# Optimization experiments

Hardware: AMD Instinct MI355X
Metric: run time of the kernel (lower is better)

## Reference

```python
import jax, jax.numpy as jnp
import numpy as np

B, S, D_IN = 2, 2048, 1024
H, DA, DH = 16, 64, 64          # num_heads, attention_dim, head_dim (linear_hidden_dim)
EMBED = 1024
KSIZE = 1


def causal_conv1d(x_bsc, w):
    """x_bsc: (B,S,Cin); w: (Cout,Cin,K). Left-pad K-1 -> causal. Returns (B,Cout,S)."""
    k = w.shape[-1]
    x_bcs = jnp.transpose(x_bsc, (0, 2, 1))
    x_bcs = jnp.pad(x_bcs, ((0, 0), (0, 0), (k - 1, 0)))
    return jax.lax.conv_general_dilated(
        x_bcs, w, window_strides=(1,), padding='VALID',
        dimension_numbers=('NCH', 'OIH', 'NCH'))


def setup_inputs() -> dict:
    key = jax.random.key(0)
    ks = jax.random.split(key, 7)
    x = jax.random.normal(ks[0], (B, S, D_IN), dtype=jnp.float32)
    # causal mask: 1 where attended, 0 where masked (masked_fill where ==0)
    attn_mask = jnp.tril(jnp.ones((S, S), dtype=jnp.int32))[None, None]  # (1,1,S,S)
    wq = 0.02 * jax.random.normal(ks[1], (H * DA, D_IN, KSIZE), dtype=jnp.float32)
    wk = 0.02 * jax.random.normal(ks[2], (H * DA, D_IN, KSIZE), dtype=jnp.float32)
    wv = 0.02 * jax.random.normal(ks[3], (H * DH, D_IN, KSIZE), dtype=jnp.float32)
    w_out = 0.02 * jax.random.normal(ks[4], (EMBED, H * DH), dtype=jnp.float32)
    b_out = 0.02 * jax.random.normal(ks[5], (EMBED,), dtype=jnp.float32)
    return {"x": x, "attn_mask": attn_mask, "wq": wq, "wk": wk, "wv": wv,
            "w_out": w_out, "b_out": b_out}


def reference(x, attn_mask, wq, wk, wv, w_out, b_out):
    b, s, _ = x.shape
    scale = DH ** (-0.5)  # NOTE: torch code scales by head_dim, not attention_dim
    q = causal_conv1d(x, wq)  # (B, H*DA, S)
    k = causal_conv1d(x, wk)  # (B, H*DA, S)
    v = causal_conv1d(x, wv)  # (B, H*DH, S)
    q = q.reshape(b, H, DA, s).transpose(0, 1, 3, 2)  # (B,H,S,DA)
    k = k.reshape(b, H, DA, s).transpose(0, 1, 3, 2)
    v = v.reshape(b, H, DH, s).transpose(0, 1, 3, 2)  # (B,H,S,DH)
    scores = scale * jnp.einsum('bhnd,bhmd->bhnm', q, k)
    scores = jnp.where(attn_mask == 0, -jnp.inf, scores)
    probs = jax.nn.softmax(scores, axis=-1)
    context = jnp.einsum('bhnm,bhmd->bhnd', probs, v)  # (B,H,S,DH)
    context = context.transpose(0, 2, 1, 3).reshape(b, s, H * DH)
    return context @ w_out.T + b_out
```

## Files before the change

kernel.cpp:

```cpp
#include <hip/hip_runtime.h>
#include <math.h>


typedef __bf16 bf16;
typedef __bf16 bf16x8 __attribute__((ext_vector_type(8)));
typedef __bf16 bf16x4 __attribute__((ext_vector_type(4)));
typedef float  f32x4  __attribute__((ext_vector_type(4)));

#define MFMA16(a, b, c) __builtin_amdgcn_mfma_f32_16x16x32_bf16((a), (b), (c), 0, 0, 0)

__device__ __forceinline__ void gll16(const void* g, void* l) {
    __builtin_amdgcn_global_load_lds(
        (__attribute__((address_space(1))) unsigned int*)g,
        (__attribute__((address_space(3))) unsigned int*)l, 16, 0, 0);
}

__global__ __launch_bounds__(256) void cvt_all_kernel(
    const float* __restrict__ x,  const float* __restrict__ wq,
    const float* __restrict__ wk, const float* __restrict__ wv,
    const float* __restrict__ wo,
    bf16* __restrict__ xb,  bf16* __restrict__ wqb, bf16* __restrict__ wkb,
    bf16* __restrict__ wvb, bf16* __restrict__ wob)
{
    const int blk = blockIdx.x;
    const float* src; bf16* dst; int off; float scale = 1.f;
    if (blk < 4096)      { src = x;  dst = xb;  off = blk * 1024; }
    else if (blk < 5120) { src = wq; dst = wqb; off = (blk - 4096) * 1024;
                           scale = 0.18033688011112042f; }
    else if (blk < 6144) { src = wk; dst = wkb; off = (blk - 5120) * 1024; }
    else if (blk < 7168) { src = wv; dst = wvb; off = (blk - 6144) * 1024; }
    else                 { src = wo; dst = wob; off = (blk - 7168) * 1024; }
    const int i = off + threadIdx.x * 4;
    f32x4 v = *(const f32x4*)(src + i);
    bf16x4 o;
    o[0] = (bf16)(v[0] * scale); o[1] = (bf16)(v[1] * scale);
    o[2] = (bf16)(v[2] * scale); o[3] = (bf16)(v[3] * scale);
    *(bf16x4*)(dst + i) = o;
}

__global__ __launch_bounds__(256, 3) void qkv_mfma_kernel(
    const bf16* __restrict__ xb, const bf16* __restrict__ wqb,
    const bf16* __restrict__ wkb, const bf16* __restrict__ wvb,
    bf16* __restrict__ Qb, bf16* __restrict__ Kb, bf16* __restrict__ Vtb)
{
    __shared__ bf16 As[2][128 * 32];
    __shared__ bf16 Bs[2][128 * 32];
    const int mt = blockIdx.x;
    const int nt = blockIdx.y;
    const int which = nt >> 3;
    const bf16* Wm = (which == 0) ? wqb : (which == 1) ? wkb : wvb;

    const int t = threadIdx.x;
    const int w = t >> 6, lane = t & 63, quad = lane >> 4, l16 = lane & 15;
    const int wm = (w >> 1) * 64, wn = (w & 1) * 64;
    const int srow = lane >> 2;
    const int scol = (lane & 3) * 8;

    const bf16* Ab = xb + ((size_t)(mt * 128) + srow) * 1024 + scol;
    const bf16* Bb = Wm + ((size_t)((nt & 7) * 128) + srow) * 1024 + scol;

    f32x4 acc[4][4];
    #pragma unroll
    for (int i = 0; i < 4; i++)
        #pragma unroll
        for (int j = 0; j < 4; j++)
            #pragma unroll
            for (int r = 0; r < 4; r++) acc[i][j][r] = 0.f;

    gll16(Ab + (size_t)(w * 16) * 1024,       As[0] + w * 512);
    gll16(Ab + (size_t)((w + 4) * 16) * 1024, As[0] + (w + 4) * 512);
    gll16(Bb + (size_t)(w * 16) * 1024,       Bs[0] + w * 512);
    gll16(Bb + (size_t)((w + 4) * 16) * 1024, Bs[0] + (w + 4) * 512);

    for (int it = 0; it < 32; it++) {
        const int cur = it & 1, nxt = cur ^ 1;
        __syncthreads();
        if (it < 31) {
            const int kn = it * 32 + 32;
            gll16(Ab + (size_t)(w * 16) * 1024 + kn,       As[nxt] + w * 512);
            gll16(Ab + (size_t)((w + 4) * 16) * 1024 + kn, As[nxt] + (w + 4) * 512);
            gll16(Bb + (size_t)(w * 16) * 1024 + kn,       Bs[nxt] + w * 512);
            gll16(Bb + (size_t)((w + 4) * 16) * 1024 + kn, Bs[nxt] + (w + 4) * 512);
        }
        bf16x8 af[4], bfr[4];
        #pragma unroll
        for (int i = 0; i < 4; i++)
            af[i] = *(const bf16x8*)&As[cur][(wm + i * 16 + l16) * 32 + quad * 8];
        #pragma unroll
        for (int j = 0; j < 4; j++)
            bfr[j] = *(const bf16x8*)&Bs[cur][(wn + j * 16 + l16) * 32 + quad * 8];
        #pragma unroll
        for (int i = 0; i < 4; i++)
            #pragma unroll
            for (int j = 0; j < 4; j++)
                acc[i][j] = MFMA16(af[i], bfr[j], acc[i][j]);
    }

    const int nbase = (nt & 7) * 128 + wn;
    if (which == 2) {
        #pragma unroll
        for (int i = 0; i < 4; i++) {
            const int m0 = mt * 128 + wm + i * 16 + quad * 4;
            const int bb = m0 >> 11, s0 = m0 & 2047;
            #pragma unroll
            for (int j = 0; j < 4; j++) {
                const int n = nbase + j * 16 + l16;
                const int h = n >> 6, d = n & 63;
                bf16x4 pk;
                #pragma unroll
                for (int r = 0; r < 4; r++) pk[r] = (bf16)acc[i][j][r];
                *(bf16x4*)&Vtb[(((size_t)(bb * 16 + h)) * 64 + d) * 2048 + s0] = pk;
            }
        }
    } else {
        bf16* Out = (which == 0) ? Qb : Kb;
        #pragma unroll
        for (int i = 0; i < 4; i++) {
            #pragma unroll
            for (int r = 0; r < 4; r++) {
                const int m = mt * 128 + wm + i * 16 + quad * 4 + r;
                const int bb = m >> 11, s = m & 2047;
                #pragma unroll
                for (int j = 0; j < 4; j++) {
                    const int n = nbase + j * 16 + l16;
                    const int h = n >> 6, d = n & 63;
                    Out[(((size_t)(bb * 16 + h)) * 2048 + s) * 64 + d] =
                        (bf16)acc[i][j][r];
                }
            }
        }
    }
}

__global__ __launch_bounds__(256, 2) void attn_mfma_kernel(
    const bf16* __restrict__ Qb, const bf16* __restrict__ Kb,
    const bf16* __restrict__ Vtb, bf16* __restrict__ ctxb)
{
    __shared__ bf16 Ks[2][128 * 64];
    __shared__ bf16 Vts[2][64 * 128];
    __shared__ bf16 Pl[4][16 * 128];

    const int id = blockIdx.x;
    const int bh = id & 31;
    const int pr = id >> 5;
    const int qa = pr, qb = 31 - pr;
    const int h = bh & 15, b = bh >> 4;
    const int t = threadIdx.x;
    const int w = t >> 6, lane = t & 63, quad = lane >> 4, l16 = lane & 15;

    const size_t hb = (size_t)(b * 16 + h);
    const bf16* Qh = Qb + hb * (2048 * 64);
    const bf16* Kh = Kb + hb * (2048 * 64);
    const bf16* Vh = Vtb + hb * (64 * 2048);

    bf16x8 qf0[2], qf1[2];
    {
        const bf16* Qr0 = Qh + (size_t)(qa * 64 + w * 16 + l16) * 64;
        qf0[0] = *(const bf16x8*)(Qr0 + quad * 8);
        qf0[1] = *(const bf16x8*)(Qr0 + 32 + quad * 8);
        const bf16* Qr1 = Qh + (size_t)(qb * 64 + w * 16 + l16) * 64;
        qf1[0] = *(const bf16x8*)(Qr1 + quad * 8);
        qf1[1] = *(const bf16x8*)(Qr1 + 32 + quad * 8);
    }

    bf16x8 ones;
    #pragma unroll
    for (int i = 0; i < 8; i++) ones[i] = (bf16)1.0f;

    f32x4 o0[4], o1[4], l0, l1;
    #pragma unroll
    for (int r = 0; r < 4; r++) { l0[r] = 0.f; l1[r] = 0.f; }
    #pragma unroll
    for (int dt = 0; dt < 4; dt++)
        #pragma unroll
        for (int r = 0; r < 4; r++) { o0[dt][r] = 0.f; o1[dt][r] = 0.f; }

    const int ksr = lane >> 3, ksc = lane & 7;
    const int vsr = lane >> 4, vsc = lane & 15;

    #define STAGE(ktv, buf)                                                   \
        {                                                                     \
            _Pragma("unroll")                                                 \
            for (int j = 0; j < 4; j++) {                                     \
                const int c = 4 * w + j;                                      \
                const int kr = c * 8 + ksr;                                   \
                gll16(Kh + (size_t)((ktv) * 128 + kr) * 64 +                  \
                          ((ksc ^ (kr & 7)) * 8),                             \
                      Ks[buf] + c * 512);                                     \
                const int vr = c * 4 + vsr;                                   \
                gll16(Vh + (size_t)vr * 2048 + (ktv) * 128 +                  \
                          ((vsc ^ (vr & 15)) * 8),                            \
                      Vts[buf] + c * 512);                                    \
            }                                                                 \
        }

    #define ITER(qt64, ktv, diag, qfv, oacc, lacc, cur)                       \
        {                                                                     \
            f32x4 sacc[8];                                                    \
            _Pragma("unroll")                                                 \
            for (int tt = 0; tt < 8; tt++) {                                  \
                _Pragma("unroll")                                             \
                for (int r = 0; r < 4; r++) sacc[tt][r] = 0.f;                \
                const int krow = tt * 16 + l16;                               \
                bf16x8 kf0 = *(const bf16x8*)&Ks[cur][krow * 64 +             \
                                 ((quad)     ^ (krow & 7)) * 8];              \
                bf16x8 kf1 = *(const bf16x8*)&Ks[cur][krow * 64 +             \
                                 ((quad + 4) ^ (krow & 7)) * 8];              \
                sacc[tt] = MFMA16(kf0, (qfv)[0], sacc[tt]);                   \
                sacc[tt] = MFMA16(kf1, (qfv)[1], sacc[tt]);                   \
            }                                                                 \
            const int qrow = (qt64) * 64 + w * 16 + l16;                      \
            _Pragma("unroll")                                                 \
            for (int tt = 0; tt < 8; tt++) {                                  \
                bf16x4 pk;                                                    \
                _Pragma("unroll")                                             \
                for (int r = 0; r < 4; r++) {                                 \
                    float p = __builtin_amdgcn_exp2f(sacc[tt][r]);            \
                    if ((diag) && ((ktv) * 128 + tt * 16 + quad * 4 + r) > qrow) \
                        p = 0.f;                                              \
                    pk[r] = (bf16)p;                                          \
                }                                                             \
                const int cs = (tt * 2 + (quad >> 1)) ^ l16;                  \
                *(bf16x4*)&Pl[w][l16 * 128 + cs * 8 + (quad & 1) * 4] = pk;   \
            }                                                                 \
            bf16x8 ap[4];                                                     \
            _Pragma("unroll")                                                 \
            for (int u = 0; u < 4; u++) {                                     \
                ap[u] = *(const bf16x8*)&Pl[w][l16 * 128 +                    \
                             ((quad + 4 * u) ^ l16) * 8];                     \
                (lacc) = MFMA16(ap[u], ones, (lacc));                         \
            }                                                                 \
            _Pragma("unroll")                                                 \
            for (int dt = 0; dt < 4; dt++) {                                  \
                const int drow = dt * 16 + l16;                               \
                _Pragma("unroll")                                             \
                for (int u = 0; u < 4; u++) {                                 \
                    bf16x8 bv = *(const bf16x8*)&Vts[cur][drow * 128 +        \
                                     ((4 * u + quad) ^ (drow & 15)) * 8];     \
                    (oacc)[dt] = MFMA16(ap[u], bv, (oacc)[dt]);               \
                }                                                             \
            }                                                                 \
        }

    const int na = (qa >> 1) + 1;
    STAGE(0, 0);

    for (int v = 0; v < 17; v++) {
        const int cur = v & 1, nxt = cur ^ 1;
        __syncthreads();
        if (v < 16) {
            const int vn = v + 1;
            const int ktn = (vn < na) ? vn : vn - na;
            STAGE(ktn, nxt);
        }
        if (v < na) {
            ITER(qa, v, (v == na - 1), qf0, o0, l0, cur);
        } else {
            const int kt = v - na;
            ITER(qb, kt, (v == 16), qf1, o1, l1, cur);
        }
    }
    #undef STAGE
    #undef ITER

    #pragma unroll
    for (int r = 0; r < 4; r++) {
        const float inv0 = 1.f / l0[r];
        const int s0 = qa * 64 + w * 16 + quad * 4 + r;
        const float inv1 = 1.f / l1[r];
        const int s1 = qb * 64 + w * 16 + quad * 4 + r;
        #pragma unroll
        for (int dt = 0; dt < 4; dt++) {
            ctxb[((size_t)(b * 2048 + s0)) * 1024 + h * 64 + dt * 16 + l16] =
                (bf16)(o0[dt][r] * inv0);
            ctxb[((size_t)(b * 2048 + s1)) * 1024 + h * 64 + dt * 16 + l16] =
                (bf16)(o1[dt][r] * inv1);
        }
    }
}

__global__ __launch_bounds__(256, 2) void oproj_mfma_kernel(
    const bf16* __restrict__ ctxb, const bf16* __restrict__ wob,
    const float* __restrict__ b_out, float* __restrict__ out)
{
    __shared__ bf16 As[2][64 * 32];
    __shared__ bf16 Bs[2][128 * 32];
    const int mt = blockIdx.x;
    const int nt = blockIdx.y;
    const int t = threadIdx.x;
    const int w = t >> 6, lane = t & 63, quad = lane >> 4, l16 = lane & 15;
    const int srow = lane >> 2;
    const int scol = (lane & 3) * 8;

    const bf16* Ab = ctxb + (size_t)(mt * 64 + srow) * 1024 + scol;
    const bf16* Bb = wob + (size_t)(nt * 128 + srow) * 1024 + scol;

    f32x4 acc[8];
    #pragma unroll
    for (int j = 0; j < 8; j++)
        #pragma unroll
        for (int r = 0; r < 4; r++) acc[j][r] = 0.f;

    gll16(Ab + (size_t)(w * 16) * 1024,       As[0] + w * 512);
    gll16(Bb + (size_t)(w * 16) * 1024,       Bs[0] + w * 512);
    gll16(Bb + (size_t)((w + 4) * 16) * 1024, Bs[0] + (w + 4) * 512);

    for (int it = 0; it < 32; it++) {
        const int cur = it & 1, nxt = cur ^ 1;
        __syncthreads();
        if (it < 31) {
            const int kn = it * 32 + 32;
            gll16(Ab + (size_t)(w * 16) * 1024 + kn,       As[nxt] + w * 512);
            gll16(Bb + (size_t)(w * 16) * 1024 + kn,       Bs[nxt] + w * 512);
            gll16(Bb + (size_t)((w + 4) * 16) * 1024 + kn, Bs[nxt] + (w + 4) * 512);
        }
        bf16x8 af = *(const bf16x8*)&As[cur][(w * 16 + l16) * 32 + quad * 8];
        #pragma unroll
        for (int j = 0; j < 8; j++) {
            bf16x8 bfr = *(const bf16x8*)&Bs[cur][(j * 16 + l16) * 32 + quad * 8];
            acc[j] = MFMA16(af, bfr, acc[j]);
        }
    }

    #pragma unroll
    for (int j = 0; j < 8; j++)
        #pragma unroll
        for (int r = 0; r < 4; r++) {
            const int m = mt * 64 + w * 16 + quad * 4 + r;
            const int n = nt * 128 + j * 16 + l16;
            out[(size_t)m * 1024 + n] = acc[j][r] + b_out[n];
        }
}

extern "C" void kernel_launch(void* const* d_in, const int* in_sizes, int n_in,
                              void* d_out, int out_size, void* d_ws, size_t ws_size,
                              hipStream_t stream)
{
    const float* x     = (const float*)d_in[0];
    const float* wq    = (const float*)d_in[2];
    const float* wk    = (const float*)d_in[3];
    const float* wv    = (const float*)d_in[4];
    const float* w_out = (const float*)d_in[5];
    const float* b_out = (const float*)d_in[6];
    float* out = (float*)d_out;

    char* ws = (char*)d_ws;
    bf16* xb   = (bf16*)(ws);
    bf16* wqb  = (bf16*)(ws + (8u  << 20));
    bf16* wkb  = (bf16*)(ws + (10u << 20));
    bf16* wvb  = (bf16*)(ws + (12u << 20));
    bf16* wob  = (bf16*)(ws + (14u << 20));
    bf16* Qb   = (bf16*)(ws + (16u << 20));
    bf16* Kb   = (bf16*)(ws + (24u << 20));
    bf16* Vtb  = (bf16*)(ws + (32u << 20));
    bf16* ctxb = (bf16*)(ws + (40u << 20));

    cvt_all_kernel<<<8192, 256, 0, stream>>>(x, wq, wk, wv, w_out,
                                             xb, wqb, wkb, wvb, wob);
    qkv_mfma_kernel<<<dim3(32, 24), 256, 0, stream>>>(xb, wqb, wkb, wvb, Qb, Kb, Vtb);
    attn_mfma_kernel<<<512, 256, 0, stream>>>(Qb, Kb, Vtb, ctxb);
    oproj_mfma_kernel<<<dim3(64, 8), 256, 0, stream>>>(ctxb, wob, b_out, out);
}
```

Baseline: 188.8 us.

## Share K/V tiles between paired query tiles and stage Q/K stores through LDS

The attention loop now walks the key tiles once, up to the longer query tile's extent. Each staged K/V tile is reused by both query tiles (qa and qb) when both need it, so the K/V loads drop from 17 stages to nb stages per block. This raises per-iteration register pressure (two score arrays) and lengthens some iterations. Separately, the QKV projection epilogue for Q/K writes the accumulators into shared memory and then emits 16-byte coalesced row stores instead of scattered 2-byte stores.

Result: no change. 192.0 us (+1.7%).

```diff
diff --git a/kernel.cpp b/kernel.cpp
--- a/kernel.cpp
+++ b/kernel.cpp
@@ -114,19 +114,24 @@
         }
     } else {
         bf16* Out = (which == 0) ? Qb : Kb;
+        bf16* Lw = ((w < 2) ? As[0] : Bs[0]) + (w & 1) * 1280;
+        const int hh = nbase >> 6;
         #pragma unroll
         for (int i = 0; i < 4; i++) {
             #pragma unroll
-            for (int r = 0; r < 4; r++) {
-                const int m = mt * 128 + wm + i * 16 + quad * 4 + r;
-                const int bb = m >> 11, s = m & 2047;
+            for (int j = 0; j < 4; j++)
                 #pragma unroll
-                for (int j = 0; j < 4; j++) {
-                    const int n = nbase + j * 16 + l16;
-                    const int h = n >> 6, d = n & 63;
-                    Out[(((size_t)(bb * 16 + h)) * 2048 + s) * 64 + d] =
-                        (bf16)acc[i][j][r];
-                }
+                for (int r = 0; r < 4; r++)
+                    Lw[(quad * 4 + r) * 72 + j * 16 + l16] = (bf16)acc[i][j][r];
+            const int m0 = mt * 128 + wm + i * 16;
+            const int bb = m0 >> 11, s0 = m0 & 2047;
+            #pragma unroll
+            for (int k = 0; k < 2; k++) {
+                const int row = k * 8 + (lane >> 3);
+                const int seg = lane & 7;
+                bf16x8 vv = *(const bf16x8*)&Lw[row * 72 + seg * 8];
+                *(bf16x8*)&Out[(((size_t)(bb * 16 + hh)) * 2048 + s0 + row) * 64 +
+                               seg * 8] = vv;
             }
         }
     }
@@ -194,28 +199,15 @@
             }                                                                 \
         }
 
-    #define ITER(qt64, ktv, diag, qfv, oacc, lacc, cur)                       \
+    #define PPHASE(qt64, ktv, diag, sacc, oacc, lacc, cur)                    \
         {                                                                     \
-            f32x4 sacc[8];                                                    \
-            _Pragma("unroll")                                                 \
-            for (int tt = 0; tt < 8; tt++) {                                  \
-                _Pragma("unroll")                                             \
-                for (int r = 0; r < 4; r++) sacc[tt][r] = 0.f;                \
-                const int krow = tt * 16 + l16;                               \
-                bf16x8 kf0 = *(const bf16x8*)&Ks[cur][krow * 64 +             \
-                                 ((quad)     ^ (krow & 7)) * 8];              \
-                bf16x8 kf1 = *(const bf16x8*)&Ks[cur][krow * 64 +             \
-                                 ((quad + 4) ^ (krow & 7)) * 8];              \
-                sacc[tt] = MFMA16(kf0, (qfv)[0], sacc[tt]);                   \
-                sacc[tt] = MFMA16(kf1, (qfv)[1], sacc[tt]);                   \
-            }                                                                 \
             const int qrow = (qt64) * 64 + w * 16 + l16;                      \
             _Pragma("unroll")                                                 \
             for (int tt = 0; tt < 8; tt++) {                                  \
                 bf16x4 pk;                                                    \
                 _Pragma("unroll")                                             \
                 for (int r = 0; r < 4; r++) {                                 \
-                    float p = __builtin_amdgcn_exp2f(sacc[tt][r]);            \
+                    float p = __builtin_amdgcn_exp2f((sacc)[tt][r]);          \
                     if ((diag) && ((ktv) * 128 + tt * 16 + quad * 4 + r) > qrow) \
                         p = 0.f;                                              \
                     pk[r] = (bf16)p;                                          \
@@ -243,25 +235,49 @@
         }
 
     const int na = (qa >> 1) + 1;
+    const int nb = (qb >> 1) + 1;
     STAGE(0, 0);
 
-    for (int v = 0; v < 17; v++) {
+    for (int v = 0; v < nb; v++) {
         const int cur = v & 1, nxt = cur ^ 1;
         __syncthreads();
-        if (v < 16) {
-            const int vn = v + 1;
-            const int ktn = (vn < na) ? vn : vn - na;
-            STAGE(ktn, nxt);
-        }
+        if (v + 1 < nb) STAGE(v + 1, nxt);
+
+        f32x4 sa[8], sb[8];
         if (v < na) {
-            ITER(qa, v, (v == na - 1), qf0, o0, l0, cur);
+            #pragma unroll
+            for (int tt = 0; tt < 8; tt++) {
+                #pragma unroll
+                for (int r = 0; r < 4; r++) { sa[tt][r] = 0.f; sb[tt][r] = 0.f; }
+                const int krow = tt * 16 + l16;
+                bf16x8 kf0 = *(const bf16x8*)&Ks[cur][krow * 64 +
+                                 ((quad)     ^ (krow & 7)) * 8];
+                bf16x8 kf1 = *(const bf16x8*)&Ks[cur][krow * 64 +
+                                 ((quad + 4) ^ (krow & 7)) * 8];
+                sa[tt] = MFMA16(kf0, qf0[0], sa[tt]);
+                sa[tt] = MFMA16(kf1, qf0[1], sa[tt]);
+                sb[tt] = MFMA16(kf0, qf1[0], sb[tt]);
+                sb[tt] = MFMA16(kf1, qf1[1], sb[tt]);
+            }
+            PPHASE(qa, v, (v == na - 1), sa, o0, l0, cur);
         } else {
-            const int kt = v - na;
-            ITER(qb, kt, (v == 16), qf1, o1, l1, cur);
-        }
+            #pragma unroll
+            for (int tt = 0; tt < 8; tt++) {
+                #pragma unroll
+                for (int r = 0; r < 4; r++) sb[tt][r] = 0.f;
+                const int krow = tt * 16 + l16;
+                bf16x8 kf0 = *(const bf16x8*)&Ks[cur][krow * 64 +
+                                 ((quad)     ^ (krow & 7)) * 8];
+                bf16x8 kf1 = *(const bf16x8*)&Ks[cur][krow * 64 +
+                                 ((quad + 4) ^ (krow & 7)) * 8];
+                sb[tt] = MFMA16(kf0, qf1[0], sb[tt]);
+                sb[tt] = MFMA16(kf1, qf1[1], sb[tt]);
+            }
+        }
+        PPHASE(qb, v, (v == nb - 1), sb, o1, l1, cur);
     }
     #undef STAGE
-    #undef ITER
+    #undef PPHASE
 
     #pragma unroll
     for (int r = 0; r < 4; r++) {
```
